# Kernel optimization log

Measured on AMD Instinct MI355X. Metric: run time of the kernel, lower is better.

Reference implementation:

```python
import jax, jax.numpy as jnp
import numpy as np

N = 10000       # num nodes
E = 320000      # num edges
F_IN = 500      # num_features
HID = 64        # hidden
C = 10          # num_classes (width of propagated signal)
RANK = 3
K = 10          # Chebyshev hops


def setup_inputs() -> dict:
    key = jax.random.key(0)
    ks = jax.random.split(key, 10)
    feature = jax.random.normal(ks[0], (N, F_IN), jnp.float32)
    src = jax.random.randint(ks[1], (E,), 0, N)
    dst = jax.random.randint(ks[2], (E,), 0, N)
    edges = jnp.stack([src, dst]).astype(jnp.int64)
    CTC = jax.random.normal(ks[3], (N, N), jnp.float32) * 0.01
    W1 = jax.random.normal(ks[4], (F_IN, HID), jnp.float32) / np.sqrt(F_IN)
    b1 = jnp.zeros((HID,), jnp.float32)
    W2 = jax.random.normal(ks[5], (HID, C), jnp.float32) / np.sqrt(HID)
    b2 = jnp.zeros((C,), jnp.float32)
    gamma = jax.random.normal(ks[6], (RANK, K + 1), jnp.float32)   # Parameter gamma
    Wp = jax.random.normal(ks[7], (K + 1, C, RANK), jnp.float32) / np.sqrt(C)  # proj_list weights (transposed)
    bp = jnp.zeros((K + 1, RANK), jnp.float32)
    return dict(feature=feature, edges=edges, CTC=CTC, W1=W1, b1=b1,
                W2=W2, b2=b2, gamma=gamma, Wp=Wp, bp=bp)


def _cheb_norm(src, dst, num_nodes):
    # remove self loops (mask to zero weight: jit-safe, mathematically identical)
    w = jnp.where(src == dst, 0.0, 1.0).astype(jnp.float32)
    deg = jax.ops.segment_sum(w, src, num_segments=num_nodes)
    dinv = jnp.where(deg > 0, 1.0 / jnp.sqrt(jnp.maximum(deg, 1e-30)), 0.0)
    # sym-normalized Laplacian: off-diag = -D^-1/2 A D^-1/2, diag = 1
    w_off = -dinv[src] * w * dinv[dst]
    lam = 2.0 * jnp.maximum(jnp.max(w_off), 1.0)  # lambda_max = 2*max(L weights); diag ones dominate
    w_off = 2.0 * w_off / lam
    diag = 2.0 / lam - 1.0  # scaled diag (2*1/lam) plus fill_value=-1 self loop, summed by scatter-add
    return w_off, diag


def reference(feature, edges, CTC, W1, b1, W2, b2, gamma, Wp, bp):
    # MLP (dropout is identity in eval mode)
    x = jax.nn.relu(feature @ W1 + b1)
    x = x @ W2 + b2  # (N, C)
    num_nodes = x.shape[0]
    src, dst = edges[0], edges[1]
    w_off, diag = _cheb_norm(src, dst, num_nodes)

    def prop(t):  # scatter-add message passing: out[i] = sum_j L_hat[i,j] t[j]
        return jax.ops.segment_sum(w_off[:, None] * t[src], dst,
                                   num_segments=num_nodes) + diag * t

    def eta(Txk, k):  # gated low-rank mixing coefficient per node
        h = jnp.tanh(Txk @ Wp[k] + bp[k])        # (N, rank)
        e = (h @ gamma[:, k]) / RANK             # (N,)
        return CTC @ e                           # (N,)

    Tx0 = x
    Tx1 = prop(Tx0)
    hidden = Tx0 * eta(Tx0, 0)[:, None] + Tx1 * eta(Tx1, 1)[:, None]
    for k in range(1, K):
        Tx2 = 2.0 * prop(Tx1) - Tx0
        Tx0, Tx1 = Tx1, Tx2
        hidden = hidden + Tx1 * eta(Tx1, k + 1)[:, None]
    return jax.nn.log_softmax(hidden, axis=1)
```

## Files before the change

### kernel.cpp

```cpp
#include <hip/hip_runtime.h>
#include <hip/hip_bf16.h>
#include <math.h>

#define NNODES 10000
#define NEDGES 320000
#define FIN    500
#define HIDN   64
#define NC     10
#define RANKP  3
#define KHOP   10
#define KP1    11

__global__ __launch_bounds__(256) void mlp_kernel(
    const float* __restrict__ feature, const float* __restrict__ W1,
    const float* __restrict__ b1, const float* __restrict__ W2,
    const float* __restrict__ b2, float* __restrict__ Tx0) {
  __shared__ float feat[4][FIN];
  __shared__ float hid[4][HIDN];
  const int t = threadIdx.x;
  const int n = t >> 6;
  const int h = t & 63;
  const int i0 = blockIdx.x * 4;

  for (int idx = t; idx < 4 * FIN; idx += 256) {
    int nn = idx / FIN, f = idx - nn * FIN;
    feat[nn][f] = feature[(size_t)(i0 + nn) * FIN + f];
  }
  __syncthreads();

  float acc = b1[h];
#pragma unroll 4
  for (int f = 0; f < FIN; ++f)
    acc = fmaf(feat[n][f], W1[f * HIDN + h], acc);
  hid[n][h] = fmaxf(acc, 0.f);
  __syncthreads();

  if (h < NC) {
    float a2 = b2[h];
#pragma unroll
    for (int k = 0; k < HIDN; ++k)
      a2 = fmaf(hid[n][k], W2[k * NC + h], a2);
    Tx0[(size_t)(i0 + n) * NC + h] = a2;
  }
}


__global__ void degcnt_kernel(const int* __restrict__ src, const int* __restrict__ dst,
                              float* __restrict__ deg, int* __restrict__ cnt) {
  int e = blockIdx.x * 256 + threadIdx.x;
  if (e >= NEDGES) return;
  int s = src[e], d = dst[e];
  if (s != d) {
    atomicAdd(&deg[s], 1.0f);
    atomicAdd(&cnt[d], 1);
  }
}

__global__ void dinv_kernel(float* __restrict__ deg) {
  int i = blockIdx.x * 256 + threadIdx.x;
  if (i >= NNODES) return;
  float dg = deg[i];
  deg[i] = (dg > 0.f) ? 1.0f / sqrtf(dg) : 0.f;
}

__global__ __launch_bounds__(256) void scan_kernel(const int* __restrict__ cnt,
                                                   int* __restrict__ row_start,
                                                   int* __restrict__ cursor) {
  const int t = threadIdx.x, lane = t & 63, w = t >> 6;
  const int CH = 40;
  const int base = t * CH;
  int sum = 0;
  for (int j = 0; j < CH; ++j) {
    int idx = base + j;
    if (idx < NNODES) sum += cnt[idx];
  }
  int inc = sum;
#pragma unroll
  for (int d = 1; d < 64; d <<= 1) {
    int u = __shfl_up(inc, d);
    if (lane >= d) inc += u;
  }
  __shared__ int wtot[4];
  if (lane == 63) wtot[w] = inc;
  __syncthreads();
  int add = 0;
  for (int i = 0; i < 4; ++i)
    if (i < w) add += wtot[i];
  int run = add + inc - sum;
  for (int j = 0; j < CH; ++j) {
    int idx = base + j;
    if (idx < NNODES) {
      int v = cnt[idx];
      row_start[idx] = run;
      cursor[idx] = run;
      run += v;
    }
  }
  if (t == 255) row_start[NNODES] = run;
}

__global__ void fill_kernel(const int* __restrict__ src, const int* __restrict__ dst,
                            const float* __restrict__ dinv, int* __restrict__ cursor,
                            int2* __restrict__ packed) {
  int e = blockIdx.x * 256 + threadIdx.x;
  if (e >= NEDGES) return;
  int s = src[e], d = dst[e];
  if (s == d) return;
  float w = -dinv[s] * dinv[d];
  int slot = atomicAdd(&cursor[d], 1);
  packed[slot] = make_int2(s, __float_as_int(w));
}

__global__ __launch_bounds__(256) void gather_kernel(
    const int* __restrict__ row_start, const int2* __restrict__ packed,
    const float* __restrict__ tin, const float* __restrict__ sub,
    float* __restrict__ tout, float scale) {
  const int g    = (blockIdx.x * 256 + threadIdx.x) >> 4;
  const int lane = threadIdx.x & 15;
  if (g >= NNODES) return;
  const int s0 = row_start[g], s1 = row_start[g + 1];
  float acc[NC];
#pragma unroll
  for (int c = 0; c < NC; ++c) acc[c] = 0.f;
  for (int j = s0 + lane; j < s1; j += 16) {
    int2 p = packed[j];
    float w = __int_as_float(p.y);
    const float2* t2 = (const float2*)(tin + (size_t)p.x * NC);
    float2 a0 = t2[0], a1 = t2[1], a2 = t2[2], a3 = t2[3], a4 = t2[4];
    acc[0] = fmaf(w, a0.x, acc[0]); acc[1] = fmaf(w, a0.y, acc[1]);
    acc[2] = fmaf(w, a1.x, acc[2]); acc[3] = fmaf(w, a1.y, acc[3]);
    acc[4] = fmaf(w, a2.x, acc[4]); acc[5] = fmaf(w, a2.y, acc[5]);
    acc[6] = fmaf(w, a3.x, acc[6]); acc[7] = fmaf(w, a3.y, acc[7]);
    acc[8] = fmaf(w, a4.x, acc[8]); acc[9] = fmaf(w, a4.y, acc[9]);
  }
#pragma unroll
  for (int c = 0; c < NC; ++c) {
    float v = acc[c];
#pragma unroll
    for (int off = 8; off > 0; off >>= 1) v += __shfl_xor(v, off);
    acc[c] = v;
  }
  if (lane == 0) {
    float* to = tout + (size_t)g * NC;
    if (sub) {
      const float* sb = sub + (size_t)g * NC;
#pragma unroll
      for (int c = 0; c < NC; ++c) to[c] = fmaf(scale, acc[c], -sb[c]);
    } else {
#pragma unroll
      for (int c = 0; c < NC; ++c) to[c] = scale * acc[c];
    }
  }
}

__global__ void proj_kernel(const float* __restrict__ Txall, const float* __restrict__ Wp,
                            const float* __restrict__ bp, const float* __restrict__ gamma,
                            float* __restrict__ Emat) {
  int i = blockIdx.x * 256 + threadIdx.x;
  if (i >= NNODES) return;
  for (int k = 0; k < KP1; ++k) {
    const float* tx = Txall + ((size_t)k * NNODES + i) * NC;
    float t[NC];
#pragma unroll
    for (int c = 0; c < NC; ++c) t[c] = tx[c];
    float e = 0.f;
#pragma unroll
    for (int r = 0; r < RANKP; ++r) {
      float hh = bp[k * RANKP + r];
#pragma unroll
      for (int c = 0; c < NC; ++c)
        hh = fmaf(t[c], Wp[(k * NC + c) * RANKP + r], hh);
      e = fmaf(tanhf(hh), gamma[r * KP1 + k], e);
    }
    Emat[(size_t)k * NNODES + i] = e * (1.0f / RANKP);
  }
}

__global__ __launch_bounds__(256) void gemv_kernel(const float* __restrict__ CTC,
                                                   const float* __restrict__ Emat,
                                                   float* __restrict__ etam) {
  const int i0 = blockIdx.x * 4;
  const int t = threadIdx.x;
  float acc[4][KP1];
#pragma unroll
  for (int r = 0; r < 4; ++r)
#pragma unroll
    for (int k = 0; k < KP1; ++k) acc[r][k] = 0.f;

  const int n4 = NNODES / 4;
  for (int j4 = t; j4 < n4; j4 += 256) {
    float4 ev[KP1];
#pragma unroll
    for (int k = 0; k < KP1; ++k)
      ev[k] = ((const float4*)(Emat + (size_t)k * NNODES))[j4];
#pragma unroll
    for (int r = 0; r < 4; ++r) {
      float4 cv = ((const float4*)(CTC + (size_t)(i0 + r) * NNODES))[j4];
#pragma unroll
      for (int k = 0; k < KP1; ++k) {
        acc[r][k] = fmaf(cv.x, ev[k].x, acc[r][k]);
        acc[r][k] = fmaf(cv.y, ev[k].y, acc[r][k]);
        acc[r][k] = fmaf(cv.z, ev[k].z, acc[r][k]);
        acc[r][k] = fmaf(cv.w, ev[k].w, acc[r][k]);
      }
    }
  }

#pragma unroll
  for (int r = 0; r < 4; ++r)
#pragma unroll
    for (int k = 0; k < KP1; ++k) {
      float v = acc[r][k];
#pragma unroll
      for (int off = 32; off > 0; off >>= 1) v += __shfl_xor(v, off);
      acc[r][k] = v;
    }
  __shared__ float red[4][4 * KP1];
  const int w = t >> 6, lane = t & 63;
  if (lane == 0) {
#pragma unroll
    for (int r = 0; r < 4; ++r)
#pragma unroll
      for (int k = 0; k < KP1; ++k) red[w][r * KP1 + k] = acc[r][k];
  }
  __syncthreads();
  if (t < 4 * KP1) {
    float s = red[0][t] + red[1][t] + red[2][t] + red[3][t];
    int r = t / KP1, k = t - r * KP1;
    etam[(size_t)(i0 + r) * KP1 + k] = s;
  }
}

__global__ void final_kernel(const float* __restrict__ Txall, const float* __restrict__ etam,
                             float* __restrict__ out) {
  int i = blockIdx.x * 256 + threadIdx.x;
  if (i >= NNODES) return;
  float eta[KP1];
#pragma unroll
  for (int k = 0; k < KP1; ++k) eta[k] = etam[(size_t)i * KP1 + k];
  float h[NC];
#pragma unroll
  for (int c = 0; c < NC; ++c) h[c] = 0.f;
  for (int k = 0; k < KP1; ++k) {
    const float* tx = Txall + ((size_t)k * NNODES + i) * NC;
#pragma unroll
    for (int c = 0; c < NC; ++c) h[c] = fmaf(tx[c], eta[k], h[c]);
  }
  float m = h[0];
#pragma unroll
  for (int c = 1; c < NC; ++c) m = fmaxf(m, h[c]);
  float s = 0.f;
#pragma unroll
  for (int c = 0; c < NC; ++c) s += expf(h[c] - m);
  float ls = logf(s);
#pragma unroll
  for (int c = 0; c < NC; ++c) out[(size_t)i * NC + c] = h[c] - m - ls;
}

extern "C" void kernel_launch(void* const* d_in, const int* in_sizes, int n_in,
                              void* d_out, int out_size, void* d_ws, size_t ws_size,
                              hipStream_t stream) {
  const float* feature = (const float*)d_in[0];
  const int*   edges   = (const int*)d_in[1];
  const float* CTC     = (const float*)d_in[2];
  const float* W1      = (const float*)d_in[3];
  const float* b1      = (const float*)d_in[4];
  const float* W2      = (const float*)d_in[5];
  const float* b2      = (const float*)d_in[6];
  const float* gamma   = (const float*)d_in[7];
  const float* Wp      = (const float*)d_in[8];
  const float* bp      = (const float*)d_in[9];
  const int* src = edges;
  const int* dst = edges + NEDGES;
  float* out = (float*)d_out;

  float* ws        = (float*)d_ws;
  float* Txall     = ws;
  float* deg       = Txall + (size_t)KP1 * NNODES * NC;
  int*   cnt       = (int*)(deg + NNODES);
  int*   row_start = cnt + NNODES;
  int*   cursor    = row_start + NNODES + 8;
  int2*  packed    = (int2*)(cursor + NNODES + 8);
  float* Emat      = (float*)(packed + NEDGES);
  float* etam      = Emat + (size_t)KP1 * NNODES;

  const int EB = (NEDGES + 255) / 256;
  const int NB = (NNODES + 255) / 256;
  const int GB = (NNODES * 16 + 255) / 256;

  hipMemsetAsync(deg, 0, 2 * NNODES * sizeof(float), stream);

  mlp_kernel<<<NNODES / 4, 256, 0, stream>>>(feature, W1, b1, W2, b2, Txall);
  degcnt_kernel<<<EB, 256, 0, stream>>>(src, dst, deg, cnt);
  dinv_kernel<<<NB, 256, 0, stream>>>(deg);
  scan_kernel<<<1, 256, 0, stream>>>(cnt, row_start, cursor);
  fill_kernel<<<EB, 256, 0, stream>>>(src, dst, deg, cursor, packed);

  float* Tx0 = Txall;
  float* Tx1 = Txall + (size_t)NNODES * NC;
  gather_kernel<<<GB, 256, 0, stream>>>(row_start, packed, Tx0, nullptr, Tx1, 1.0f);
  for (int k = 1; k < KHOP; ++k) {
    float* prev = Txall + (size_t)(k - 1) * NNODES * NC;
    float* cur  = Txall + (size_t)k * NNODES * NC;
    float* nxt  = Txall + (size_t)(k + 1) * NNODES * NC;
    gather_kernel<<<GB, 256, 0, stream>>>(row_start, packed, cur, prev, nxt, 2.0f);
  }

  proj_kernel<<<NB, 256, 0, stream>>>(Txall, Wp, bp, gamma, Emat);
  gemv_kernel<<<NNODES / 4, 256, 0, stream>>>(CTC, Emat, etam);
  final_kernel<<<NB, 256, 0, stream>>>(Txall, etam, out);
}
```

Measured before the change: 812.4 us.

## Fuse MLP, Chebyshev propagation and projection into one cooperative kernel

Replaces the MLP, the ten gather launches and the projection kernel with one persistent cooperative kernel of 512 blocks. The stages are separated by grid-wide syncs, which removes per-launch overhead and the gaps between kernels. The degree inverse-sqrt is folded into the edge fill kernel, and the eta gemv is merged with the final combine and log-softmax, which drops the intermediate eta buffer. In exchange there are eleven grid barriers, the MLP now reads feature rows straight from global memory with fewer blocks instead of staging them in shared memory, and launch bounds cap occupancy at two blocks per CU.

Result: slower. 1.495 ms (+84.0%).

```diff
diff --git a/kernel.cpp b/kernel.cpp
--- a/kernel.cpp
+++ b/kernel.cpp
@@ -1,6 +1,9 @@
 #include <hip/hip_runtime.h>
 #include <hip/hip_bf16.h>
+#include <hip/hip_cooperative_groups.h>
 #include <math.h>
+
+namespace cg = cooperative_groups;
 
 #define NNODES 10000
 #define NEDGES 320000
@@ -10,39 +13,8 @@
 #define RANKP  3
 #define KHOP   10
 #define KP1    11
-
-__global__ __launch_bounds__(256) void mlp_kernel(
-    const float* __restrict__ feature, const float* __restrict__ W1,
-    const float* __restrict__ b1, const float* __restrict__ W2,
-    const float* __restrict__ b2, float* __restrict__ Tx0) {
-  __shared__ float feat[4][FIN];
-  __shared__ float hid[4][HIDN];
-  const int t = threadIdx.x;
-  const int n = t >> 6;
-  const int h = t & 63;
-  const int i0 = blockIdx.x * 4;
-
-  for (int idx = t; idx < 4 * FIN; idx += 256) {
-    int nn = idx / FIN, f = idx - nn * FIN;
-    feat[nn][f] = feature[(size_t)(i0 + nn) * FIN + f];
-  }
-  __syncthreads();
-
-  float acc = b1[h];
-#pragma unroll 4
-  for (int f = 0; f < FIN; ++f)
-    acc = fmaf(feat[n][f], W1[f * HIDN + h], acc);
-  hid[n][h] = fmaxf(acc, 0.f);
-  __syncthreads();
-
-  if (h < NC) {
-    float a2 = b2[h];
-#pragma unroll
-    for (int k = 0; k < HIDN; ++k)
-      a2 = fmaf(hid[n][k], W2[k * NC + h], a2);
-    Tx0[(size_t)(i0 + n) * NC + h] = a2;
-  }
-}
+#define CBLKS  512
+#define NGRP   (CBLKS * 16)
 
 
 __global__ void degcnt_kernel(const int* __restrict__ src, const int* __restrict__ dst,
@@ -54,13 +26,6 @@
     atomicAdd(&deg[s], 1.0f);
     atomicAdd(&cnt[d], 1);
   }
-}
-
-__global__ void dinv_kernel(float* __restrict__ deg) {
-  int i = blockIdx.x * 256 + threadIdx.x;
-  if (i >= NNODES) return;
-  float dg = deg[i];
-  deg[i] = (dg > 0.f) ? 1.0f / sqrtf(dg) : 0.f;
 }
 
 __global__ __launch_bounds__(256) void scan_kernel(const int* __restrict__ cnt,
@@ -100,85 +65,136 @@
 }
 
 __global__ void fill_kernel(const int* __restrict__ src, const int* __restrict__ dst,
-                            const float* __restrict__ dinv, int* __restrict__ cursor,
+                            const float* __restrict__ deg, int* __restrict__ cursor,
                             int2* __restrict__ packed) {
   int e = blockIdx.x * 256 + threadIdx.x;
   if (e >= NEDGES) return;
   int s = src[e], d = dst[e];
   if (s == d) return;
-  float w = -dinv[s] * dinv[d];
+  float ds_ = deg[s], dd = deg[d];
+  float dis = (ds_ > 0.f) ? 1.0f / sqrtf(ds_) : 0.f;
+  float did = (dd  > 0.f) ? 1.0f / sqrtf(dd)  : 0.f;
+  float w = -dis * did;
   int slot = atomicAdd(&cursor[d], 1);
   packed[slot] = make_int2(s, __float_as_int(w));
 }
 
-__global__ __launch_bounds__(256) void gather_kernel(
-    const int* __restrict__ row_start, const int2* __restrict__ packed,
-    const float* __restrict__ tin, const float* __restrict__ sub,
-    float* __restrict__ tout, float scale) {
-  const int g    = (blockIdx.x * 256 + threadIdx.x) >> 4;
-  const int lane = threadIdx.x & 15;
-  if (g >= NNODES) return;
-  const int s0 = row_start[g], s1 = row_start[g + 1];
-  float acc[NC];
-#pragma unroll
-  for (int c = 0; c < NC; ++c) acc[c] = 0.f;
-  for (int j = s0 + lane; j < s1; j += 16) {
-    int2 p = packed[j];
-    float w = __int_as_float(p.y);
-    const float2* t2 = (const float2*)(tin + (size_t)p.x * NC);
-    float2 a0 = t2[0], a1 = t2[1], a2 = t2[2], a3 = t2[3], a4 = t2[4];
-    acc[0] = fmaf(w, a0.x, acc[0]); acc[1] = fmaf(w, a0.y, acc[1]);
-    acc[2] = fmaf(w, a1.x, acc[2]); acc[3] = fmaf(w, a1.y, acc[3]);
-    acc[4] = fmaf(w, a2.x, acc[4]); acc[5] = fmaf(w, a2.y, acc[5]);
-    acc[6] = fmaf(w, a3.x, acc[6]); acc[7] = fmaf(w, a3.y, acc[7]);
-    acc[8] = fmaf(w, a4.x, acc[8]); acc[9] = fmaf(w, a4.y, acc[9]);
-  }
-#pragma unroll
-  for (int c = 0; c < NC; ++c) {
-    float v = acc[c];
-#pragma unroll
-    for (int off = 8; off > 0; off >>= 1) v += __shfl_xor(v, off);
-    acc[c] = v;
-  }
-  if (lane == 0) {
-    float* to = tout + (size_t)g * NC;
-    if (sub) {
-      const float* sb = sub + (size_t)g * NC;
-#pragma unroll
-      for (int c = 0; c < NC; ++c) to[c] = fmaf(scale, acc[c], -sb[c]);
-    } else {
-#pragma unroll
-      for (int c = 0; c < NC; ++c) to[c] = scale * acc[c];
-    }
-  }
-}
-
-__global__ void proj_kernel(const float* __restrict__ Txall, const float* __restrict__ Wp,
-                            const float* __restrict__ bp, const float* __restrict__ gamma,
-                            float* __restrict__ Emat) {
-  int i = blockIdx.x * 256 + threadIdx.x;
-  if (i >= NNODES) return;
-  for (int k = 0; k < KP1; ++k) {
-    const float* tx = Txall + ((size_t)k * NNODES + i) * NC;
-    float t[NC];
-#pragma unroll
-    for (int c = 0; c < NC; ++c) t[c] = tx[c];
-    float e = 0.f;
-#pragma unroll
-    for (int r = 0; r < RANKP; ++r) {
-      float hh = bp[k * RANKP + r];
-#pragma unroll
-      for (int c = 0; c < NC; ++c)
-        hh = fmaf(t[c], Wp[(k * NC + c) * RANKP + r], hh);
-      e = fmaf(tanhf(hh), gamma[r * KP1 + k], e);
-    }
-    Emat[(size_t)k * NNODES + i] = e * (1.0f / RANKP);
-  }
-}
-
-__global__ __launch_bounds__(256) void gemv_kernel(const float* __restrict__ CTC,
-                                                   const float* __restrict__ Emat,
-                                                   float* __restrict__ etam) {
+__global__ __launch_bounds__(256, 2) void coop_kernel(
+    const float* __restrict__ feature, const float* __restrict__ W1,
+    const float* __restrict__ b1, const float* __restrict__ W2,
+    const float* __restrict__ b2, const int* __restrict__ row_start,
+    const int2* __restrict__ packed, const float* __restrict__ Wp,
+    const float* __restrict__ bp, const float* __restrict__ gamma,
+    float* __restrict__ Txall, float* __restrict__ Emat) {
+  cg::grid_group grid = cg::this_grid();
+  const int t = threadIdx.x;
+  const int b = blockIdx.x;
+
+  __shared__ float hid[16][HIDN + 1];
+  {
+    const int w = t >> 6, lane = t & 63;
+    for (int pass = 0; pass < 2; ++pass) {
+      const int base = pass * NGRP + b * 16;
+      for (int nn = w * 4; nn < w * 4 + 4; ++nn) {
+        const int node = base + nn;
+        float acc0 = b1[lane], acc1 = 0.f;
+        if (node < NNODES) {
+          const float* frow = feature + (size_t)node * FIN;
+          for (int f = 0; f < FIN; f += 2) {
+            acc0 = fmaf(frow[f],     W1[f * HIDN + lane],       acc0);
+            acc1 = fmaf(frow[f + 1], W1[(f + 1) * HIDN + lane], acc1);
+          }
+        }
+        hid[nn][lane] = fmaxf(acc0 + acc1, 0.f);
+      }
+      __syncthreads();
+      if (t < 16 * NC) {
+        const int nn = t / NC, c = t - nn * NC;
+        const int node = base + nn;
+        if (node < NNODES) {
+          float a2 = b2[c];
+#pragma unroll
+          for (int k2 = 0; k2 < HIDN; ++k2)
+            a2 = fmaf(hid[nn][k2], W2[k2 * NC + c], a2);
+          Txall[(size_t)node * NC + c] = a2;
+        }
+      }
+      __syncthreads();
+    }
+  }
+  grid.sync();
+
+  const int grp = t >> 4, lane16 = t & 15;
+  const int gid = b * 16 + grp;
+  for (int step = 1; step <= KHOP; ++step) {
+    const float* tin  = Txall + (size_t)(step - 1) * NNODES * NC;
+    const float* sub  = (step >= 2) ? Txall + (size_t)(step - 2) * NNODES * NC
+                                    : nullptr;
+    float*       tout = Txall + (size_t)step * NNODES * NC;
+    const float scale = (step >= 2) ? 2.f : 1.f;
+    for (int node = gid; node < NNODES; node += NGRP) {
+      const int s0 = row_start[node], s1 = row_start[node + 1];
+      float acc[NC];
+#pragma unroll
+      for (int c = 0; c < NC; ++c) acc[c] = 0.f;
+      for (int j = s0 + lane16; j < s1; j += 16) {
+        int2 p = packed[j];
+        float w = __int_as_float(p.y);
+        const float2* t2 = (const float2*)(tin + (size_t)p.x * NC);
+        float2 a0 = t2[0], a1 = t2[1], a2 = t2[2], a3 = t2[3], a4 = t2[4];
+        acc[0] = fmaf(w, a0.x, acc[0]); acc[1] = fmaf(w, a0.y, acc[1]);
+        acc[2] = fmaf(w, a1.x, acc[2]); acc[3] = fmaf(w, a1.y, acc[3]);
+        acc[4] = fmaf(w, a2.x, acc[4]); acc[5] = fmaf(w, a2.y, acc[5]);
+        acc[6] = fmaf(w, a3.x, acc[6]); acc[7] = fmaf(w, a3.y, acc[7]);
+        acc[8] = fmaf(w, a4.x, acc[8]); acc[9] = fmaf(w, a4.y, acc[9]);
+      }
+#pragma unroll
+      for (int c = 0; c < NC; ++c) {
+        float v = acc[c];
+#pragma unroll
+        for (int off = 8; off > 0; off >>= 1) v += __shfl_xor(v, off);
+        acc[c] = v;
+      }
+      if (lane16 == 0) {
+        float* to = tout + (size_t)node * NC;
+        if (sub) {
+          const float* sb = sub + (size_t)node * NC;
+#pragma unroll
+          for (int c = 0; c < NC; ++c) to[c] = fmaf(scale, acc[c], -sb[c]);
+        } else {
+#pragma unroll
+          for (int c = 0; c < NC; ++c) to[c] = acc[c];
+        }
+      }
+    }
+    grid.sync();
+  }
+
+  {
+    const int idx = b * 256 + t;
+    if (idx < NNODES * KP1) {
+      const int k = idx / NNODES, i = idx - k * NNODES;
+      const float* tx = Txall + ((size_t)k * NNODES + i) * NC;
+      float tv[NC];
+#pragma unroll
+      for (int c = 0; c < NC; ++c) tv[c] = tx[c];
+      float e = 0.f;
+#pragma unroll
+      for (int r = 0; r < RANKP; ++r) {
+        float hh = bp[k * RANKP + r];
+#pragma unroll
+        for (int c = 0; c < NC; ++c)
+          hh = fmaf(tv[c], Wp[(k * NC + c) * RANKP + r], hh);
+        e = fmaf(tanhf(hh), gamma[r * KP1 + k], e);
+      }
+      Emat[(size_t)k * NNODES + i] = e * (1.0f / RANKP);
+    }
+  }
+}
+
+__global__ __launch_bounds__(256) void gemv_final_kernel(
+    const float* __restrict__ CTC, const float* __restrict__ Emat,
+    const float* __restrict__ Txall, float* __restrict__ out) {
   const int i0 = blockIdx.x * 4;
   const int t = threadIdx.x;
   float acc[4][KP1];
@@ -225,36 +241,30 @@
   }
   __syncthreads();
   if (t < 4 * KP1) {
-    float s = red[0][t] + red[1][t] + red[2][t] + red[3][t];
-    int r = t / KP1, k = t - r * KP1;
-    etam[(size_t)(i0 + r) * KP1 + k] = s;
-  }
-}
-
-__global__ void final_kernel(const float* __restrict__ Txall, const float* __restrict__ etam,
-                             float* __restrict__ out) {
-  int i = blockIdx.x * 256 + threadIdx.x;
-  if (i >= NNODES) return;
-  float eta[KP1];
-#pragma unroll
-  for (int k = 0; k < KP1; ++k) eta[k] = etam[(size_t)i * KP1 + k];
-  float h[NC];
-#pragma unroll
-  for (int c = 0; c < NC; ++c) h[c] = 0.f;
-  for (int k = 0; k < KP1; ++k) {
-    const float* tx = Txall + ((size_t)k * NNODES + i) * NC;
-#pragma unroll
-    for (int c = 0; c < NC; ++c) h[c] = fmaf(tx[c], eta[k], h[c]);
-  }
-  float m = h[0];
-#pragma unroll
-  for (int c = 1; c < NC; ++c) m = fmaxf(m, h[c]);
-  float s = 0.f;
-#pragma unroll
-  for (int c = 0; c < NC; ++c) s += expf(h[c] - m);
-  float ls = logf(s);
-#pragma unroll
-  for (int c = 0; c < NC; ++c) out[(size_t)i * NC + c] = h[c] - m - ls;
+    red[0][t] = red[0][t] + red[1][t] + red[2][t] + red[3][t];
+  }
+  __syncthreads();
+  if (t < 4) {
+    const int node = i0 + t;
+    float h[NC];
+#pragma unroll
+    for (int c = 0; c < NC; ++c) h[c] = 0.f;
+    for (int k = 0; k < KP1; ++k) {
+      const float e = red[0][t * KP1 + k];
+      const float* tx = Txall + ((size_t)k * NNODES + node) * NC;
+#pragma unroll
+      for (int c = 0; c < NC; ++c) h[c] = fmaf(tx[c], e, h[c]);
+    }
+    float m = h[0];
+#pragma unroll
+    for (int c = 1; c < NC; ++c) m = fmaxf(m, h[c]);
+    float s = 0.f;
+#pragma unroll
+    for (int c = 0; c < NC; ++c) s += expf(h[c] - m);
+    const float ls = logf(s);
+#pragma unroll
+    for (int c = 0; c < NC; ++c) out[(size_t)node * NC + c] = h[c] - m - ls;
+  }
 }
 
 extern "C" void kernel_launch(void* const* d_in, const int* in_sizes, int n_in,
@@ -282,31 +292,20 @@
   int*   cursor    = row_start + NNODES + 8;
   int2*  packed    = (int2*)(cursor + NNODES + 8);
   float* Emat      = (float*)(packed + NEDGES);
-  float* etam      = Emat + (size_t)KP1 * NNODES;
 
   const int EB = (NEDGES + 255) / 256;
-  const int NB = (NNODES + 255) / 256;
-  const int GB = (NNODES * 16 + 255) / 256;
 
   hipMemsetAsync(deg, 0, 2 * NNODES * sizeof(float), stream);
 
-  mlp_kernel<<<NNODES / 4, 256, 0, stream>>>(feature, W1, b1, W2, b2, Txall);
   degcnt_kernel<<<EB, 256, 0, stream>>>(src, dst, deg, cnt);
-  dinv_kernel<<<NB, 256, 0, stream>>>(deg);
   scan_kernel<<<1, 256, 0, stream>>>(cnt, row_start, cursor);
   fill_kernel<<<EB, 256, 0, stream>>>(src, dst, deg, cursor, packed);
 
-  float* Tx0 = Txall;
-  float* Tx1 = Txall + (size_t)NNODES * NC;
-  gather_kernel<<<GB, 256, 0, stream>>>(row_start, packed, Tx0, nullptr, Tx1, 1.0f);
-  for (int k = 1; k < KHOP; ++k) {
-    float* prev = Txall + (size_t)(k - 1) * NNODES * NC;
-    float* cur  = Txall + (size_t)k * NNODES * NC;
-    float* nxt  = Txall + (size_t)(k + 1) * NNODES * NC;
-    gather_kernel<<<GB, 256, 0, stream>>>(row_start, packed, cur, prev, nxt, 2.0f);
-  }
-
-  proj_kernel<<<NB, 256, 0, stream>>>(Txall, Wp, bp, gamma, Emat);
-  gemv_kernel<<<NNODES / 4, 256, 0, stream>>>(CTC, Emat, etam);
-  final_kernel<<<NB, 256, 0, stream>>>(Txall, etam, out);
-}
+  void* cargs[] = {(void*)&feature, (void*)&W1, (void*)&b1, (void*)&W2,
+                   (void*)&b2, (void*)&row_start, (void*)&packed, (void*)&Wp,
+                   (void*)&bp, (void*)&gamma, (void*)&Txall, (void*)&Emat};
+  hipLaunchCooperativeKernel((const void*)coop_kernel, dim3(CBLKS), dim3(256),
+                             cargs, 0, stream);
+
+  gemv_final_kernel<<<NNODES / 4, 256, 0, stream>>>(CTC, Emat, Txall, out);
+}
```
